# Kernel tuning notes

Measured on AMD Instinct MI355X. Metric: run time of the kernel, lower is better.

Reference implementation:

```python
import jax, jax.numpy as jnp
import numpy as np

QUANT_RANGE = 8
HALF_RANGE = QUANT_RANGE // 2  # 4, i.e. int4-style symmetric clamp [-4, 3]


def _find_zero_scale(t):
    zero = t.min()
    scale = (t.max() - zero) / (2 * HALF_RANGE)
    return zero, scale


def _quantize(t):
    zero, scale = _find_zero_scale(t)
    q = jnp.clip((t - zero) / scale - HALF_RANGE, -HALF_RANGE, HALF_RANGE - 1).astype(jnp.int32)
    return q, zero, scale


def setup_inputs() -> dict:
    key = jax.random.key(0)
    k1, k2, k3 = jax.random.split(key, 3)
    in_features = 4096
    out_features = 4096
    batch = 4096  # must equal out_features (shift broadcast in original module)
    x = jax.random.normal(k1, (batch, in_features), dtype=jnp.float32)
    # kaiming_uniform_(a=sqrt(5)) -> bound = 1/sqrt(in_features)
    bound = 1.0 / np.sqrt(in_features)
    weight = jax.random.uniform(k2, (out_features, in_features), dtype=jnp.float32,
                                minval=-bound, maxval=bound)
    bias = jax.random.uniform(k3, (out_features,), dtype=jnp.float32,
                              minval=-bound, maxval=bound)
    return {"x": x, "weight": weight, "bias": bias}


def reference(x, weight, bias):
    # Quantize activations and weights with global affine (min/max) quant.
    x_q, zero_act, scale_act = _quantize(x)          # [B, in], scalars
    w_q, _, _ = _quantize(weight)                    # [out, in]
    # Integer-valued GEMM (done in fp32, matching F.linear on .float() casts).
    result = x_q.astype(jnp.float32) @ w_q.astype(jnp.float32).T + bias  # [B, out]
    # Dequantize with weight-row-sum shift.
    scale_weight = (weight.max() - weight.min()) / (2 * HALF_RANGE)
    weights_reduced = weight.sum(axis=1)             # [out]
    shift = (zero_act + HALF_RANGE * scale_act) * weights_reduced[:, None]  # [out, 1]
    # NOTE: original torch code broadcasts [B,out] + [out,1]; requires B == out.
    return result * scale_act * scale_weight + shift
```

## Files before the change

### kernel.cpp

```cpp
#include <hip/hip_runtime.h>
#include <stdint.h>


using i32x4  = __attribute__((ext_vector_type(4))) int;
using i32x16 = __attribute__((ext_vector_type(16))) int;

#define TID ((int)threadIdx.x)

__global__ __launch_bounds__(256) void k_stats(const float4* __restrict__ x,
                                               const float4* __restrict__ w,
                                               float* __restrict__ pmin,
                                               float* __restrict__ pmax,
                                               float* __restrict__ wsum) {
  const int blk = blockIdx.x;
  const bool isw = blk < 4096;
  const float4* src = isw ? (w + (size_t)blk * 1024)
                          : (x + (size_t)(blk - 4096) * 1024);
  float4 v0 = src[TID], v1 = src[256 + TID], v2 = src[512 + TID], v3 = src[768 + TID];
  float lmin = fminf(fminf(fminf(v0.x, v0.y), fminf(v0.z, v0.w)),
                     fminf(fminf(v1.x, v1.y), fminf(v1.z, v1.w)));
  lmin = fminf(lmin, fminf(fminf(fminf(v2.x, v2.y), fminf(v2.z, v2.w)),
                           fminf(fminf(v3.x, v3.y), fminf(v3.z, v3.w))));
  float lmax = fmaxf(fmaxf(fmaxf(v0.x, v0.y), fmaxf(v0.z, v0.w)),
                     fmaxf(fmaxf(v1.x, v1.y), fmaxf(v1.z, v1.w)));
  lmax = fmaxf(lmax, fmaxf(fmaxf(fmaxf(v2.x, v2.y), fmaxf(v2.z, v2.w)),
                           fmaxf(fmaxf(v3.x, v3.y), fmaxf(v3.z, v3.w))));
  float lsum = ((v0.x + v0.y) + (v0.z + v0.w)) + ((v1.x + v1.y) + (v1.z + v1.w)) +
               ((v2.x + v2.y) + (v2.z + v2.w)) + ((v3.x + v3.y) + (v3.z + v3.w));

#pragma unroll
  for (int d = 32; d > 0; d >>= 1) {
    lmin = fminf(lmin, __shfl_down(lmin, d));
    lmax = fmaxf(lmax, __shfl_down(lmax, d));
    lsum += __shfl_down(lsum, d);
  }
  __shared__ float smn[4], smx[4], ssm[4];
  const int wv = TID >> 6;
  if ((TID & 63) == 0) { smn[wv] = lmin; smx[wv] = lmax; ssm[wv] = lsum; }
  __syncthreads();
  if (TID == 0) {
    float mn = fminf(fminf(smn[0], smn[1]), fminf(smn[2], smn[3]));
    float mx = fmaxf(fmaxf(smx[0], smx[1]), fmaxf(smx[2], smx[3]));
    pmin[blk] = mn; pmax[blk] = mx;
    if (isw) wsum[blk] = (ssm[0] + ssm[1]) + (ssm[2] + ssm[3]);
  }
}

__global__ __launch_bounds__(256) void k_final(const float* __restrict__ pmin,
                                               const float* __restrict__ pmax,
                                               float* __restrict__ mmf) {
  float wmn = 1e30f, wmx = -1e30f, xmn = 1e30f, xmx = -1e30f;
  for (int i = TID; i < 4096; i += 256) {
    wmn = fminf(wmn, pmin[i]);        wmx = fmaxf(wmx, pmax[i]);
    xmn = fminf(xmn, pmin[4096 + i]); xmx = fmaxf(xmx, pmax[4096 + i]);
  }
#pragma unroll
  for (int d = 32; d > 0; d >>= 1) {
    xmn = fminf(xmn, __shfl_down(xmn, d));
    xmx = fmaxf(xmx, __shfl_down(xmx, d));
    wmn = fminf(wmn, __shfl_down(wmn, d));
    wmx = fmaxf(wmx, __shfl_down(wmx, d));
  }
  __shared__ float s[4][4];
  const int wv = TID >> 6;
  if ((TID & 63) == 0) { s[wv][0] = xmn; s[wv][1] = xmx; s[wv][2] = wmn; s[wv][3] = wmx; }
  __syncthreads();
  if (TID == 0) {
    mmf[0] = fminf(fminf(s[0][0], s[1][0]), fminf(s[2][0], s[3][0]));
    mmf[1] = fmaxf(fmaxf(s[0][1], s[1][1]), fmaxf(s[2][1], s[3][1]));
    mmf[2] = fminf(fminf(s[0][2], s[1][2]), fminf(s[2][2], s[3][2]));
    mmf[3] = fmaxf(fmaxf(s[0][3], s[1][3]), fmaxf(s[2][3], s[3][3]));
  }
}

__device__ __forceinline__ int q1i(float t, float zero, float scale) {
  float v = (t - zero) / scale - 4.0f;
  v = fminf(3.0f, fmaxf(-4.0f, v));
  return (int)v;
}

__device__ __forceinline__ unsigned pack4(float4 v, float zero, float scale) {
  return (q1i(v.x, zero, scale) & 255) | ((q1i(v.y, zero, scale) & 255) << 8) |
         ((q1i(v.z, zero, scale) & 255) << 16) | ((q1i(v.w, zero, scale) & 255) << 24);
}

__global__ __launch_bounds__(256) void k_quant(const float4* __restrict__ x,
                                               const float4* __restrict__ w,
                                               uint4* __restrict__ Xq,
                                               uint4* __restrict__ Wq,
                                               const float* __restrict__ mmf) {
  bool isx = (blockIdx.x < 4096);
  int row = isx ? blockIdx.x : (blockIdx.x - 4096);
  const float4* in = (isx ? x : w) + (size_t)row * 1024 + TID * 4;
  uint4* outq = (isx ? Xq : Wq) + (size_t)row * 256 + TID;
  float zero = isx ? mmf[0] : mmf[2];
  float scale = ((isx ? mmf[1] : mmf[3]) - zero) * 0.125f;
  float4 a = in[0], b = in[1], c = in[2], d = in[3];
  uint4 o;
  o.x = pack4(a, zero, scale);
  o.y = pack4(b, zero, scale);
  o.z = pack4(c, zero, scale);
  o.w = pack4(d, zero, scale);
  *outq = o;
}

__device__ __forceinline__ void gload_lds16(const char* g, char* l) {
  __builtin_amdgcn_global_load_lds(
      (__attribute__((address_space(1))) void*)(g),
      (__attribute__((address_space(3))) void*)(l), 16, 0, 0);
}

__global__ __launch_bounds__(256, 2) void k_gemm(const char* __restrict__ Xq,
                                                 const char* __restrict__ Wq,
                                                 const float* __restrict__ bias,
                                                 const float* __restrict__ wsum,
                                                 const float* __restrict__ mmf,
                                                 float* __restrict__ out) {
  __shared__ __align__(16) char As[256 * 128];
  __shared__ __align__(16) char Bs[128 * 128];

  const int tid = TID;
  const int bx = blockIdx.x, by = blockIdx.y;
  const int lane = tid & 63, wave = tid >> 6;
  const int wm = (wave >> 1) * 128, wn = (wave & 1) * 64;
  const int c5 = lane & 31, h = lane >> 5, s7 = c5 & 7;

  const int lc = (tid & 7) ^ ((tid >> 3) & 7);
  const char* gA = Xq + (size_t)(by * 256 + (tid >> 3)) * 4096 + lc * 16;
  const char* gB = Wq + (size_t)(bx * 128 + (tid >> 3)) * 4096 + lc * 16;
  char* lA = As + tid * 16;
  char* lB = Bs + tid * 16;

  const i32x4* As4 = (const i32x4*)As;
  const i32x4* Bs4 = (const i32x4*)Bs;

  i32x16 acc[4][2];
#pragma unroll
  for (int i = 0; i < 4; ++i)
#pragma unroll
    for (int j = 0; j < 2; ++j)
#pragma unroll
      for (int e = 0; e < 16; ++e) acc[i][j][e] = 0;

  for (int k0 = 0; k0 < 4096; k0 += 128) {
#pragma unroll
    for (int s = 0; s < 8; ++s)
      gload_lds16(gA + (size_t)s * 32 * 4096, lA + s * 4096);
#pragma unroll
    for (int s = 0; s < 4; ++s)
      gload_lds16(gB + (size_t)s * 32 * 4096, lB + s * 4096);
    gA += 128; gB += 128;
    __syncthreads();

#pragma unroll
    for (int kt = 0; kt < 4; ++kt) {
      const int ch = (kt * 2 + h) ^ s7;
      i32x4 af[4], bf[2];
#pragma unroll
      for (int i = 0; i < 4; ++i) af[i] = As4[(wm + i * 32 + c5) * 8 + ch];
#pragma unroll
      for (int j = 0; j < 2; ++j) bf[j] = Bs4[(wn + j * 32 + c5) * 8 + ch];
#pragma unroll
      for (int i = 0; i < 4; ++i)
#pragma unroll
        for (int j = 0; j < 2; ++j)
          acc[i][j] = __builtin_amdgcn_mfma_i32_32x32x32_i8(af[i], bf[j], acc[i][j], 0, 0, 0);
    }
    __syncthreads();
  }

  float sa = (mmf[1] - mmf[0]) * 0.125f;
  float sw = (mmf[3] - mmf[2]) * 0.125f;
  float mid = mmf[0] + 4.0f * sa;

  const int col0 = bx * 128 + wn + c5;
  const float b0 = bias[col0], b1 = bias[col0 + 32];
#pragma unroll
  for (int i = 0; i < 4; ++i) {
    const int rbase = by * 256 + wm + i * 32 + 4 * h;
#pragma unroll
    for (int g = 0; g < 4; ++g) {
#pragma unroll
      for (int q = 0; q < 4; ++q) {
        const int row = rbase + 8 * g + q;
        const float sh = mid * wsum[row];
        float* po = out + (size_t)row * 4096 + col0;
        po[0]  = ((float)acc[i][0][g * 4 + q] + b0) * sa * sw + sh;
        po[32] = ((float)acc[i][1][g * 4 + q] + b1) * sa * sw + sh;
      }
    }
  }
}

extern "C" void kernel_launch(void* const* d_in, const int* in_sizes, int n_in,
                              void* d_out, int out_size, void* d_ws, size_t ws_size,
                              hipStream_t stream) {
  (void)in_sizes; (void)n_in; (void)out_size; (void)ws_size;
  const float* x = (const float*)d_in[0];
  const float* w = (const float*)d_in[1];
  const float* bias = (const float*)d_in[2];
  float* out = (float*)d_out;

  char* ws = (char*)d_ws;
  float* mmf = (float*)ws;
  float* wsum = (float*)(ws + 1024);
  float* pmin = (float*)(ws + 32768);
  float* pmax = (float*)(ws + 65536);
  char* Xq = ws + 131072;
  char* Wq = ws + 131072 + (size_t)16777216;

  k_stats<<<8192, 256, 0, stream>>>((const float4*)x, (const float4*)w, pmin, pmax, wsum);
  k_final<<<1, 256, 0, stream>>>(pmin, pmax, mmf);
  k_quant<<<8192, 256, 0, stream>>>((const float4*)x, (const float4*)w,
                                    (uint4*)Xq, (uint4*)Wq, mmf);
  dim3 g(32, 16);
  k_gemm<<<g, 256, 0, stream>>>(Xq, Wq, bias, wsum, mmf, out);
}
```

Baseline: 253.8 us.

## Rewrite int8 GEMM as 256x256 double-buffered pipelined tile with 8 waves

The GEMM kernel moves to 512 threads per block, each computing a 256x256 output tile over a single 128KB LDS buffer split into double-buffered A/B stages. Global-to-LDS loads for the next K step are issued inside each MFMA phase, with explicit vmcnt waits, barriers and raised wave priority around the MFMA groups, so loads overlap compute. A swizzled 1D block ordering is meant to improve L2 reuse across neighbouring blocks. The large LDS footprint limits the kernel to one block per CU, and the hand-written wait counts are fragile if the compiler reorders memory operations.

```diff
diff --git a/kernel.cpp b/kernel.cpp
--- a/kernel.cpp
+++ b/kernel.cpp
@@ -110,29 +110,28 @@
       (__attribute__((address_space(3))) void*)(l), 16, 0, 0);
 }
 
-__global__ __launch_bounds__(256, 2) void k_gemm(const char* __restrict__ Xq,
+__global__ __launch_bounds__(512, 2) void k_gemm(const char* __restrict__ Xq,
                                                  const char* __restrict__ Wq,
                                                  const float* __restrict__ bias,
                                                  const float* __restrict__ wsum,
                                                  const float* __restrict__ mmf,
                                                  float* __restrict__ out) {
-  __shared__ __align__(16) char As[256 * 128];
-  __shared__ __align__(16) char Bs[128 * 128];
+  __shared__ __align__(16) char LDS[131072];
 
   const int tid = TID;
-  const int bx = blockIdx.x, by = blockIdx.y;
   const int lane = tid & 63, wave = tid >> 6;
-  const int wm = (wave >> 1) * 128, wn = (wave & 1) * 64;
-  const int c5 = lane & 31, h = lane >> 5, s7 = c5 & 7;
-
-  const int lc = (tid & 7) ^ ((tid >> 3) & 7);
-  const char* gA = Xq + (size_t)(by * 256 + (tid >> 3)) * 4096 + lc * 16;
-  const char* gB = Wq + (size_t)(bx * 128 + (tid >> 3)) * 4096 + lc * 16;
-  char* lA = As + tid * 16;
-  char* lB = Bs + tid * 16;
-
-  const i32x4* As4 = (const i32x4*)As;
-  const i32x4* Bs4 = (const i32x4*)Bs;
+  const int c5 = lane & 31, h = lane >> 5;
+  const int wm = (wave >> 2) * 128, wn = (wave & 3) * 64;
+
+  const int bid = (int)blockIdx.x;
+  const int swz = (bid & 7) * 32 + (bid >> 3);
+  const int bx = swz & 15, by = swz >> 4;
+  const int brow = by * 256, bcol = bx * 256;
+
+  const int srow = tid >> 2;
+  const int lcg = (tid & 3) ^ (srow & 3);
+  const char* gA = Xq + (size_t)(brow + srow) * 4096 + lcg * 16;
+  const char* gB = Wq + (size_t)(bcol + srow) * 4096 + lcg * 16;
 
   i32x16 acc[4][2];
 #pragma unroll
@@ -142,51 +141,98 @@
 #pragma unroll
       for (int e = 0; e < 16; ++e) acc[i][j][e] = 0;
 
-  for (int k0 = 0; k0 < 4096; k0 += 128) {
-#pragma unroll
-    for (int s = 0; s < 8; ++s)
-      gload_lds16(gA + (size_t)s * 32 * 4096, lA + s * 4096);
-#pragma unroll
-    for (int s = 0; s < 4; ++s)
-      gload_lds16(gB + (size_t)s * 32 * 4096, lB + s * 4096);
-    gA += 128; gB += 128;
-    __syncthreads();
-
-#pragma unroll
-    for (int kt = 0; kt < 4; ++kt) {
-      const int ch = (kt * 2 + h) ^ s7;
-      i32x4 af[4], bf[2];
-#pragma unroll
-      for (int i = 0; i < 4; ++i) af[i] = As4[(wm + i * 32 + c5) * 8 + ch];
-#pragma unroll
-      for (int j = 0; j < 2; ++j) bf[j] = Bs4[(wn + j * 32 + c5) * 8 + ch];
-#pragma unroll
-      for (int i = 0; i < 4; ++i)
-#pragma unroll
-        for (int j = 0; j < 2; ++j)
-          acc[i][j] = __builtin_amdgcn_mfma_i32_32x32x32_i8(af[i], bf[j], acc[i][j], 0, 0, 0);
+#pragma unroll
+  for (int s = 0; s < 8; ++s) {
+    const int kk = s >> 2, arr = (s >> 1) & 1, sh = s & 1;
+    const char* gs = arr ? gB : gA;
+    gload_lds16(gs + (size_t)kk * 64 + (size_t)sh * (128 * 4096),
+                LDS + arr * 65536 + kk * 16384 + sh * 8192 + tid * 16);
+  }
+  asm volatile("s_waitcnt vmcnt(4)" ::: "memory");
+  __builtin_amdgcn_s_barrier();
+
+#pragma unroll 2
+  for (int it = 0; it < 31; ++it) {
+    const int cur = it & 1, nxt = cur ^ 1;
+    const int curA = cur * 32768, curB = 65536 + cur * 32768;
+    const int nxtA = nxt * 32768, nxtB = 65536 + nxt * 32768;
+    const size_t kOff = (size_t)(2 * it + 2) * 64;
+#pragma unroll
+    for (int ph = 0; ph < 4; ++ph) {
+      const int kk = ph >> 1, ktl = ph & 1;
+      const int pco = ((ktl * 2 + h) ^ (c5 & 3)) * 16;
+      const int ab = curA + kk * 16384 + pco;
+      const int bb = curB + kk * 16384 + pco;
+      i32x4 af0 = *(const i32x4*)(LDS + ab + (wm + c5) * 64);
+      i32x4 af1 = *(const i32x4*)(LDS + ab + (wm + 32 + c5) * 64);
+      i32x4 af2 = *(const i32x4*)(LDS + ab + (wm + 64 + c5) * 64);
+      i32x4 af3 = *(const i32x4*)(LDS + ab + (wm + 96 + c5) * 64);
+      i32x4 bf0 = *(const i32x4*)(LDS + bb + (wn + c5) * 64);
+      i32x4 bf1 = *(const i32x4*)(LDS + bb + (wn + 32 + c5) * 64);
+      const char* gs = ktl ? gB : gA;
+      char* ld = LDS + (ktl ? nxtB : nxtA) + kk * 16384 + tid * 16;
+      gload_lds16(gs + kOff + (size_t)kk * 64, ld);
+      gload_lds16(gs + kOff + (size_t)kk * 64 + (size_t)(128 * 4096), ld + 8192);
+      if (ktl) asm volatile("s_waitcnt vmcnt(4)" ::: "memory");
+      __builtin_amdgcn_s_barrier();
+      asm volatile("s_waitcnt lgkmcnt(0)" ::: "memory");
+      __builtin_amdgcn_sched_barrier(0);
+      __builtin_amdgcn_s_setprio(1);
+      acc[0][0] = __builtin_amdgcn_mfma_i32_32x32x32_i8(af0, bf0, acc[0][0], 0, 0, 0);
+      acc[0][1] = __builtin_amdgcn_mfma_i32_32x32x32_i8(af0, bf1, acc[0][1], 0, 0, 0);
+      acc[1][0] = __builtin_amdgcn_mfma_i32_32x32x32_i8(af1, bf0, acc[1][0], 0, 0, 0);
+      acc[1][1] = __builtin_amdgcn_mfma_i32_32x32x32_i8(af1, bf1, acc[1][1], 0, 0, 0);
+      acc[2][0] = __builtin_amdgcn_mfma_i32_32x32x32_i8(af2, bf0, acc[2][0], 0, 0, 0);
+      acc[2][1] = __builtin_amdgcn_mfma_i32_32x32x32_i8(af2, bf1, acc[2][1], 0, 0, 0);
+      acc[3][0] = __builtin_amdgcn_mfma_i32_32x32x32_i8(af3, bf0, acc[3][0], 0, 0, 0);
+      acc[3][1] = __builtin_amdgcn_mfma_i32_32x32x32_i8(af3, bf1, acc[3][1], 0, 0, 0);
+      __builtin_amdgcn_s_setprio(0);
+      __builtin_amdgcn_s_barrier();
     }
-    __syncthreads();
+  }
+
+  asm volatile("s_waitcnt vmcnt(0)" ::: "memory");
+  __builtin_amdgcn_s_barrier();
+#pragma unroll
+  for (int ph = 0; ph < 4; ++ph) {
+    const int kk = ph >> 1, ktl = ph & 1;
+    const int pco = ((ktl * 2 + h) ^ (c5 & 3)) * 16;
+    const int ab = 32768 + kk * 16384 + pco;
+    const int bb = 98304 + kk * 16384 + pco;
+    i32x4 af0 = *(const i32x4*)(LDS + ab + (wm + c5) * 64);
+    i32x4 af1 = *(const i32x4*)(LDS + ab + (wm + 32 + c5) * 64);
+    i32x4 af2 = *(const i32x4*)(LDS + ab + (wm + 64 + c5) * 64);
+    i32x4 af3 = *(const i32x4*)(LDS + ab + (wm + 96 + c5) * 64);
+    i32x4 bf0 = *(const i32x4*)(LDS + bb + (wn + c5) * 64);
+    i32x4 bf1 = *(const i32x4*)(LDS + bb + (wn + 32 + c5) * 64);
+    acc[0][0] = __builtin_amdgcn_mfma_i32_32x32x32_i8(af0, bf0, acc[0][0], 0, 0, 0);
+    acc[0][1] = __builtin_amdgcn_mfma_i32_32x32x32_i8(af0, bf1, acc[0][1], 0, 0, 0);
+    acc[1][0] = __builtin_amdgcn_mfma_i32_32x32x32_i8(af1, bf0, acc[1][0], 0, 0, 0);
+    acc[1][1] = __builtin_amdgcn_mfma_i32_32x32x32_i8(af1, bf1, acc[1][1], 0, 0, 0);
+    acc[2][0] = __builtin_amdgcn_mfma_i32_32x32x32_i8(af2, bf0, acc[2][0], 0, 0, 0);
+    acc[2][1] = __builtin_amdgcn_mfma_i32_32x32x32_i8(af2, bf1, acc[2][1], 0, 0, 0);
+    acc[3][0] = __builtin_amdgcn_mfma_i32_32x32x32_i8(af3, bf0, acc[3][0], 0, 0, 0);
+    acc[3][1] = __builtin_amdgcn_mfma_i32_32x32x32_i8(af3, bf1, acc[3][1], 0, 0, 0);
   }
 
   float sa = (mmf[1] - mmf[0]) * 0.125f;
   float sw = (mmf[3] - mmf[2]) * 0.125f;
   float mid = mmf[0] + 4.0f * sa;
 
-  const int col0 = bx * 128 + wn + c5;
+  const int col0 = bcol + wn + c5;
   const float b0 = bias[col0], b1 = bias[col0 + 32];
 #pragma unroll
   for (int i = 0; i < 4; ++i) {
-    const int rbase = by * 256 + wm + i * 32 + 4 * h;
+    const int rbase = brow + wm + i * 32 + 4 * h;
 #pragma unroll
     for (int g = 0; g < 4; ++g) {
 #pragma unroll
       for (int q = 0; q < 4; ++q) {
         const int row = rbase + 8 * g + q;
-        const float sh = mid * wsum[row];
+        const float shift = mid * wsum[row];
         float* po = out + (size_t)row * 4096 + col0;
-        po[0]  = ((float)acc[i][0][g * 4 + q] + b0) * sa * sw + sh;
-        po[32] = ((float)acc[i][1][g * 4 + q] + b1) * sa * sw + sh;
+        po[0]  = ((float)acc[i][0][g * 4 + q] + b0) * sa * sw + shift;
+        po[32] = ((float)acc[i][1][g * 4 + q] + b1) * sa * sw + shift;
       }
     }
   }
@@ -213,6 +259,5 @@
   k_final<<<1, 256, 0, stream>>>(pmin, pmax, mmf);
   k_quant<<<8192, 256, 0, stream>>>((const float4*)x, (const float4*)w,
                                     (uint4*)Xq, (uint4*)Wq, mmf);
-  dim3 g(32, 16);
-  k_gemm<<<g, 256, 0, stream>>>(Xq, Wq, bias, wsum, mmf, out);
-}
+  k_gemm<<<256, 512, 0, stream>>>(Xq, Wq, bias, wsum, mmf, out);
+}
```

Result: slower. 259.5 us (+2.3%).
